# Performance work log

Hardware: AMD Instinct MI355X
Metric: run time of the kernel (lower is better)

## Reference

```python
import jax, jax.numpy as jnp
import numpy as np

B, S, D, H = 2, 2048, 1024, 16
HD = D // H  # head_dim = 64


def setup_inputs() -> dict:
    key = jax.random.key(0)
    ks = jax.random.split(key, 5)
    scale = 1.0 / np.sqrt(D)
    return {
        "x": jax.random.normal(ks[0], (B, S, D), dtype=jnp.float32),
        "attention_mask": jnp.zeros((B, 1, 1, S), dtype=jnp.float32),
        "Wq": jax.random.normal(ks[1], (D, D), dtype=jnp.float32) * scale,
        "Wk": jax.random.normal(ks[2], (D, D), dtype=jnp.float32) * scale,
        "Wv": jax.random.normal(ks[3], (D, D), dtype=jnp.float32) * scale,
        "Wo": jax.random.normal(ks[4], (D, D), dtype=jnp.float32) * scale,
    }


def reference(x, attention_mask, Wq, Wk, Wv, Wo):
    # nn.Linear applies x @ W.T; weights here stored as [out, in]
    q = jnp.einsum("bsd,ed->bse", x, Wq).reshape(B, S, H, HD).transpose(0, 2, 1, 3)
    k = jnp.einsum("bsd,ed->bse", x, Wk).reshape(B, S, H, HD).transpose(0, 2, 1, 3)
    v = jnp.einsum("bsd,ed->bse", x, Wv).reshape(B, S, H, HD).transpose(0, 2, 1, 3)
    scores = jnp.einsum("bhqd,bhkd->bhqk", q, k) / jnp.sqrt(jnp.float32(HD))
    scores = scores + attention_mask  # additive mask, broadcasts [B,1,1,S]
    attn = jax.nn.softmax(scores, axis=-1)  # dropout p=0 (eval) -> identity
    ctx = jnp.einsum("bhqk,bhkd->bhqd", attn, v)
    ctx = ctx.transpose(0, 2, 1, 3).reshape(B, S, D)
    out = jnp.einsum("bsd,ed->bse", ctx, Wo)
    return out
```

## Files before the change

### kernel.cpp

```cpp
#include <hip/hip_runtime.h>
#include <hip/hip_bf16.h>
#include <cstdint>
#include <cstddef>


#define B_  2
#define S_  2048
#define D_  1024
#define H_  16
#define HD_ 64

typedef __bf16 bf16x8 __attribute__((ext_vector_type(8)));
typedef __bf16 bf16x4 __attribute__((ext_vector_type(4)));
typedef float  f32x4  __attribute__((ext_vector_type(4)));

__device__ __forceinline__ void async16(const __bf16* g, const __bf16* l) {
  __builtin_amdgcn_global_load_lds(
      (const __attribute__((address_space(1))) void*)(uintptr_t)g,
      (__attribute__((address_space(3))) void*)(uint32_t)(uintptr_t)l,
      16, 0, 0);
}

__device__ __forceinline__ unsigned cvt_pk_bf16(float lo, float hi) {
  unsigned r;
  asm("v_cvt_pk_bf16_f32 %0, %1, %2" : "=v"(r) : "v"(lo), "v"(hi));
  return r;
}

__global__ __launch_bounds__(256) void cvt_all(const float* __restrict__ x,
    const float* __restrict__ wq, const float* __restrict__ wk,
    const float* __restrict__ wv, const float* __restrict__ wo,
    __bf16* __restrict__ xb, __bf16* __restrict__ wqb, __bf16* __restrict__ wkb,
    __bf16* __restrict__ wvb, __bf16* __restrict__ wob) {
  const int sel = blockIdx.y;
  const float* src; __bf16* dst; int n;
  if      (sel == 0) { src = x;  dst = xb;  n = B_ * S_ * D_; }
  else if (sel == 1) { src = wq; dst = wqb; n = D_ * D_; }
  else if (sel == 2) { src = wk; dst = wkb; n = D_ * D_; }
  else if (sel == 3) { src = wv; dst = wvb; n = D_ * D_; }
  else               { src = wo; dst = wob; n = D_ * D_; }
  for (int i = blockIdx.x * 256 + threadIdx.x; i * 4 < n; i += gridDim.x * 256) {
    const float4 v = *(const float4*)(src + (size_t)i * 4);
    bf16x4 o;
    o[0] = (__bf16)v.x; o[1] = (__bf16)v.y; o[2] = (__bf16)v.z; o[3] = (__bf16)v.w;
    *(bf16x4*)(dst + (size_t)i * 4) = o;
  }
}

template <typename TC>
__device__ __forceinline__ void gemm97_body(const __bf16* __restrict__ A,
                                            const __bf16* __restrict__ Bm,
                                            TC* __restrict__ C,
                                            const int m0, const int n0,
                                            const int N, const int K) {
  __shared__ __align__(16) __bf16 As[128 * 64];
  __shared__ __align__(16) __bf16 Bs[128 * 64];
  const int tid  = threadIdx.x, lane = tid & 63, wave = tid >> 6;
  const int l15  = lane & 15,   quad = lane >> 4;
  const int wr   = wave >> 1,   wc   = wave & 1;
  const int ebase = wave * 2048 + lane * 8;

  f32x4 acc[4][4] = {};
  for (int k0 = 0; k0 < K; k0 += 64) {
#pragma unroll
    for (int i = 0; i < 4; ++i) {
      const int e = ebase + i * 512;
      const int row = e >> 6, col = e & 63;
      async16(A  + (size_t)(m0 + row) * K + k0 + col, As + (wave * 4 + i) * 512);
      async16(Bm + (size_t)(n0 + row) * K + k0 + col, Bs + (wave * 4 + i) * 512);
    }
    __syncthreads();
#pragma unroll
    for (int kk = 0; kk < 2; ++kk) {
      bf16x8 af[4], bfv[4];
#pragma unroll
      for (int rt = 0; rt < 4; ++rt)
        af[rt] = *(const bf16x8*)(As + (wr * 64 + rt * 16 + l15) * 64 + kk * 32 + quad * 8);
#pragma unroll
      for (int ct = 0; ct < 4; ++ct)
        bfv[ct] = *(const bf16x8*)(Bs + (wc * 64 + ct * 16 + l15) * 64 + kk * 32 + quad * 8);
#pragma unroll
      for (int rt = 0; rt < 4; ++rt)
#pragma unroll
        for (int ct = 0; ct < 4; ++ct)
          acc[rt][ct] = __builtin_amdgcn_mfma_f32_16x16x32_bf16(af[rt], bfv[ct], acc[rt][ct], 0, 0, 0);
    }
    __syncthreads();
  }
#pragma unroll
  for (int rt = 0; rt < 4; ++rt)
#pragma unroll
    for (int ct = 0; ct < 4; ++ct)
#pragma unroll
      for (int r = 0; r < 4; ++r) {
        const int row = m0 + wr * 64 + rt * 16 + quad * 4 + r;
        const int col = n0 + wc * 64 + ct * 16 + l15;
        C[(size_t)row * N + col] = (TC)acc[rt][ct][r];
      }
}

__global__ __launch_bounds__(256) void qkv_gemm(const __bf16* __restrict__ xb,
                                                const __bf16* __restrict__ wq,
                                                const __bf16* __restrict__ wk,
                                                const __bf16* __restrict__ wv,
                                                __bf16* __restrict__ qkv) {
  const int sel = blockIdx.x >> 3;
  const __bf16* Bm = (sel == 0) ? wq : (sel == 1) ? wk : wv;
  __bf16* C = qkv + (size_t)sel * ((size_t)B_ * S_ * D_);
  gemm97_body<__bf16>(xb, Bm, C, blockIdx.y * 128, (blockIdx.x & 7) * 128, D_, D_);
}

__global__ __launch_bounds__(256) void o_gemm(const __bf16* __restrict__ cb,
                                              const __bf16* __restrict__ wo,
                                              float* __restrict__ out) {
  gemm97_body<float>(cb, wo, out, blockIdx.y * 128, blockIdx.x * 128, D_, D_);
}

__global__ __launch_bounds__(256) void vtrans(const __bf16* __restrict__ vb,
                                              __bf16* __restrict__ vt) {
  __shared__ __bf16 tbuf[64][72];
  const int tid = threadIdx.x;
  const int s0 = blockIdx.x * 64, bh = blockIdx.y;
  const int b = bh >> 4, h = bh & 15;
  const __bf16* src = vb + ((size_t)b * S_ + s0) * D_ + h * HD_;
#pragma unroll
  for (int i = 0; i < 2; ++i) {
    const int r = i * 32 + (tid >> 3), c8 = (tid & 7) * 8;
    *(bf16x8*)(&tbuf[r][c8]) = *(const bf16x8*)(src + (size_t)r * D_ + c8);
  }
  __syncthreads();
  __bf16* dst = vt + (size_t)bh * HD_ * S_ + s0;
#pragma unroll
  for (int i = 0; i < 2; ++i) {
    const int hd = i * 32 + (tid >> 3), sc = (tid & 7) * 8;
    bf16x8 v;
#pragma unroll
    for (int j = 0; j < 8; ++j) v[j] = tbuf[sc + j][hd];
    *(bf16x8*)(dst + (size_t)hd * S_ + sc) = v;
  }
}

__global__ __launch_bounds__(512, 4) void attn2(const __bf16* __restrict__ Q,
                                                const __bf16* __restrict__ K,
                                                const __bf16* __restrict__ Vt,
                                                const float* __restrict__ mask,
                                                __bf16* __restrict__ O) {
  constexpr int LKT = 72, LVT = 136;
  __shared__ __align__(16) __bf16 kt[128 * LKT];
  __shared__ __align__(16) __bf16 vt[64 * LVT];
  __shared__ __align__(16) float  msk[128];

  const int tid  = threadIdx.x, lane = tid & 63, wave = tid >> 6;
  const int l15  = lane & 15,   quad = lane >> 4;
  const int b = blockIdx.z, h = blockIdx.y, q0 = blockIdx.x * 128;
  const size_t base   = (size_t)b * S_ * D_ + h * HD_;
  const size_t vtbase = (size_t)(b * H_ + h) * HD_ * S_;
  const int qw = q0 + wave * 16;
  constexpr float LOG2E = 1.44269504088896340736f;
  constexpr float SC    = 0.125f * LOG2E;

  bf16x8 qf[2];
#pragma unroll
  for (int kb = 0; kb < 2; ++kb)
    qf[kb] = *(const bf16x8*)(Q + base + (size_t)(qw + l15) * D_ + kb * 32 + quad * 8);

  float m_run = -1e30f, l_run = 0.f;
  f32x4 oacc[4] = {};

  for (int t0 = 0; t0 < S_; t0 += 128) {
    __syncthreads();
#pragma unroll
    for (int i = 0; i < 2; ++i) {
      const int idx = i * 512 + tid;
      { const int row = idx >> 3, c8 = (idx & 7) * 8;
        *(bf16x8*)(kt + row * LKT + c8) =
            *(const bf16x8*)(K + base + (size_t)(t0 + row) * D_ + c8); }
      { const int row = idx >> 4, c8 = (idx & 15) * 8;
        *(bf16x8*)(vt + row * LVT + c8) =
            *(const bf16x8*)(Vt + vtbase + (size_t)row * S_ + t0 + c8); }
    }
    if (tid < 128) msk[tid] = mask[(size_t)b * S_ + t0 + tid] * LOG2E;
    __syncthreads();

    f32x4 sacc[8] = {};
    __builtin_amdgcn_s_setprio(1);
#pragma unroll
    for (int kti = 0; kti < 8; ++kti) {
      const __bf16* kr = kt + (kti * 16 + l15) * LKT + quad * 8;
      const bf16x8 a0 = *(const bf16x8*)(kr);
      const bf16x8 a1 = *(const bf16x8*)(kr + 32);
      sacc[kti] = __builtin_amdgcn_mfma_f32_16x16x32_bf16(a0, qf[0], sacc[kti], 0, 0, 0);
      sacc[kti] = __builtin_amdgcn_mfma_f32_16x16x32_bf16(a1, qf[1], sacc[kti], 0, 0, 0);
    }
    __builtin_amdgcn_s_setprio(0);

    f32x4 tm4;
#pragma unroll
    for (int r = 0; r < 4; ++r) tm4[r] = -1e30f;
#pragma unroll
    for (int kti = 0; kti < 8; ++kti) {
      const f32x4 mv = *(const f32x4*)(msk + kti * 16 + quad * 4);
#pragma unroll
      for (int r = 0; r < 4; ++r) {
        sacc[kti][r] = sacc[kti][r] * SC + mv[r];
        tm4[r] = fmaxf(tm4[r], sacc[kti][r]);
      }
    }
    float tm = fmaxf(fmaxf(tm4[0], tm4[1]), fmaxf(tm4[2], tm4[3]));
    tm = fmaxf(tm, __shfl_xor(tm, 16));
    tm = fmaxf(tm, __shfl_xor(tm, 32));

    if (!__all(tm <= m_run + 8.f)) {
      const float mnew  = fmaxf(m_run, tm);
      const float alpha = __builtin_amdgcn_exp2f(m_run - mnew);
      m_run = mnew;
      l_run *= alpha;
#pragma unroll
      for (int r = 0; r < 4; ++r) {
        const float aR = __shfl(alpha, quad * 4 + r);
#pragma unroll
        for (int nt = 0; nt < 4; ++nt) oacc[nt][r] *= aR;
      }
    }

    float ts = 0.f;
#pragma unroll
    for (int kb = 0; kb < 4; ++kb) {
      unsigned dd[2][2];
#pragma unroll
      for (int kk = 0; kk < 2; ++kk) {
        const int kti = 2 * kb + kk;
        float p[4];
#pragma unroll
        for (int r = 0; r < 4; ++r) {
          p[r] = __builtin_amdgcn_exp2f(sacc[kti][r] - m_run);
          ts += p[r];
        }
        dd[kk][0] = cvt_pk_bf16(p[0], p[1]);
        dd[kk][1] = cvt_pk_bf16(p[2], p[3]);
      }
      unsigned a0 = dd[0][0], b0 = dd[1][0], a1 = dd[0][1], b1 = dd[1][1];
      asm("v_permlane32_swap_b32 %0, %1" : "+v"(a0), "+v"(b0));
      asm("v_permlane16_swap_b32 %0, %1" : "+v"(a0), "+v"(b0));
      asm("v_permlane32_swap_b32 %0, %1" : "+v"(a1), "+v"(b1));
      asm("v_permlane16_swap_b32 %0, %1" : "+v"(a1), "+v"(b1));
      union { unsigned u[4]; bf16x8 v; } pw;
      pw.u[0] = a0; pw.u[1] = a1; pw.u[2] = b0; pw.u[3] = b1;
      const bf16x8 pa = pw.v;
      __builtin_amdgcn_s_setprio(1);
#pragma unroll
      for (int nt = 0; nt < 4; ++nt) {
        const bf16x8 vf = *(const bf16x8*)(vt + (nt * 16 + l15) * LVT + kb * 32 + quad * 8);
        oacc[nt] = __builtin_amdgcn_mfma_f32_16x16x32_bf16(pa, vf, oacc[nt], 0, 0, 0);
      }
      __builtin_amdgcn_s_setprio(0);
    }
    ts += __shfl_xor(ts, 16);
    ts += __shfl_xor(ts, 32);
    l_run += ts;
  }

#pragma unroll
  for (int r = 0; r < 4; ++r) {
    const float lR  = __shfl(l_run, quad * 4 + r);
    const float inv = 1.0f / lR;
    const int row = qw + quad * 4 + r;
#pragma unroll
    for (int nt = 0; nt < 4; ++nt)
      O[base + (size_t)row * D_ + nt * 16 + l15] = (__bf16)(oacc[nt][r] * inv);
  }
}

extern "C" void kernel_launch(void* const* d_in, const int* in_sizes, int n_in,
                              void* d_out, int out_size, void* d_ws, size_t ws_size,
                              hipStream_t stream) {
  const float* x    = (const float*)d_in[0];
  const float* mask = (const float*)d_in[1];
  const float* Wq   = (const float*)d_in[2];
  const float* Wk   = (const float*)d_in[3];
  const float* Wv   = (const float*)d_in[4];
  const float* Wo   = (const float*)d_in[5];

  char* ws = (char*)d_ws;
  const size_t MB = 1ull << 20;
  const size_t NT = (size_t)B_ * S_ * D_;
  __bf16* xb  = (__bf16*)(ws);
  __bf16* wqb = (__bf16*)(ws + 8 * MB);
  __bf16* wkb = (__bf16*)(ws + 10 * MB);
  __bf16* wvb = (__bf16*)(ws + 12 * MB);
  __bf16* wob = (__bf16*)(ws + 14 * MB);
  __bf16* qkv = (__bf16*)(ws + 16 * MB);
  __bf16* qb  = qkv;
  __bf16* kb  = qkv + NT;
  __bf16* vb  = qkv + 2 * NT;
  __bf16* vtb = xb;
  __bf16* cb  = vb;

  cvt_all<<<dim3(1024, 5), 256, 0, stream>>>(x, Wq, Wk, Wv, Wo, xb, wqb, wkb, wvb, wob);
  qkv_gemm<<<dim3(24, 32), 256, 0, stream>>>(xb, wqb, wkb, wvb, qkv);
  vtrans<<<dim3(32, 32), 256, 0, stream>>>(vb, vtb);
  attn2<<<dim3(S_ / 128, H_, B_), 512, 0, stream>>>(qb, kb, vtb, mask, cb);
  o_gemm<<<dim3(8, 32), 256, 0, stream>>>(cb, wob, (float*)d_out);
}
```

Before: 226.9 us.

## Double-buffer K/V tiles with register prefetch and compute row sums via MFMA

```diff
diff --git a/kernel.cpp b/kernel.cpp
--- a/kernel.cpp
+++ b/kernel.cpp
@@ -146,9 +146,9 @@
                                                 const float* __restrict__ mask,
                                                 __bf16* __restrict__ O) {
   constexpr int LKT = 72, LVT = 136;
-  __shared__ __align__(16) __bf16 kt[128 * LKT];
-  __shared__ __align__(16) __bf16 vt[64 * LVT];
-  __shared__ __align__(16) float  msk[128];
+  __shared__ __align__(16) __bf16 kt[2][128 * LKT];
+  __shared__ __align__(16) __bf16 vt[2][64 * LVT];
+  __shared__ __align__(16) float  mfull[S_];
 
   const int tid  = threadIdx.x, lane = tid & 63, wave = tid >> 6;
   const int l15  = lane & 15,   quad = lane >> 4;
@@ -158,35 +158,59 @@
   const int qw = q0 + wave * 16;
   constexpr float LOG2E = 1.44269504088896340736f;
   constexpr float SC    = 0.125f * LOG2E;
+  constexpr int  NT     = S_ / 128;
+
+  const int idx0 = tid,        kr0 = idx0 >> 3, kc0 = (idx0 & 7) * 8;
+  const int idx1 = 512 + tid,  kr1 = idx1 >> 3, kc1 = (idx1 & 7) * 8;
+  const int vr0 = idx0 >> 4, vc0 = (idx0 & 15) * 8;
+  const int vr1 = idx1 >> 4, vc1 = (idx1 & 15) * 8;
 
   bf16x8 qf[2];
 #pragma unroll
   for (int kb = 0; kb < 2; ++kb)
     qf[kb] = *(const bf16x8*)(Q + base + (size_t)(qw + l15) * D_ + kb * 32 + quad * 8);
 
-  float m_run = -1e30f, l_run = 0.f;
+  bf16x8 ones;
+#pragma unroll
+  for (int j = 0; j < 8; ++j) ones[j] = (__bf16)1.0f;
+
+  float m_run = -1e30f;
   f32x4 oacc[4] = {};
-
-  for (int t0 = 0; t0 < S_; t0 += 128) {
-    __syncthreads();
-#pragma unroll
-    for (int i = 0; i < 2; ++i) {
-      const int idx = i * 512 + tid;
-      { const int row = idx >> 3, c8 = (idx & 7) * 8;
-        *(bf16x8*)(kt + row * LKT + c8) =
-            *(const bf16x8*)(K + base + (size_t)(t0 + row) * D_ + c8); }
-      { const int row = idx >> 4, c8 = (idx & 15) * 8;
-        *(bf16x8*)(vt + row * LVT + c8) =
-            *(const bf16x8*)(Vt + vtbase + (size_t)row * S_ + t0 + c8); }
-    }
-    if (tid < 128) msk[tid] = mask[(size_t)b * S_ + t0 + tid] * LOG2E;
-    __syncthreads();
+  f32x4 lacc   = {};
+
+  bf16x8 rk0, rk1, rv0, rv1;
+  rk0 = *(const bf16x8*)(K + base + (size_t)kr0 * D_ + kc0);
+  rk1 = *(const bf16x8*)(K + base + (size_t)kr1 * D_ + kc1);
+  rv0 = *(const bf16x8*)(Vt + vtbase + (size_t)vr0 * S_ + vc0);
+  rv1 = *(const bf16x8*)(Vt + vtbase + (size_t)vr1 * S_ + vc1);
+#pragma unroll
+  for (int i = 0; i < S_ / 512; ++i)
+    mfull[i * 512 + tid] = mask[(size_t)b * S_ + i * 512 + tid] * LOG2E;
+  *(bf16x8*)(&kt[0][kr0 * LKT + kc0]) = rk0;
+  *(bf16x8*)(&kt[0][kr1 * LKT + kc1]) = rk1;
+  *(bf16x8*)(&vt[0][vr0 * LVT + vc0]) = rv0;
+  *(bf16x8*)(&vt[0][vr1 * LVT + vc1]) = rv1;
+  __syncthreads();
+
+  for (int t = 0; t < NT; ++t) {
+    const int cur = t & 1;
+    const int t0  = t * 128;
+    const __bf16* ktb = &kt[cur][0];
+    const __bf16* vtb = &vt[cur][0];
+
+    if (t + 1 < NT) {
+      const int tn = t0 + 128;
+      rk0 = *(const bf16x8*)(K + base + (size_t)(tn + kr0) * D_ + kc0);
+      rk1 = *(const bf16x8*)(K + base + (size_t)(tn + kr1) * D_ + kc1);
+      rv0 = *(const bf16x8*)(Vt + vtbase + (size_t)vr0 * S_ + tn + vc0);
+      rv1 = *(const bf16x8*)(Vt + vtbase + (size_t)vr1 * S_ + tn + vc1);
+    }
 
     f32x4 sacc[8] = {};
     __builtin_amdgcn_s_setprio(1);
 #pragma unroll
     for (int kti = 0; kti < 8; ++kti) {
-      const __bf16* kr = kt + (kti * 16 + l15) * LKT + quad * 8;
+      const __bf16* kr = ktb + (kti * 16 + l15) * LKT + quad * 8;
       const bf16x8 a0 = *(const bf16x8*)(kr);
       const bf16x8 a1 = *(const bf16x8*)(kr + 32);
       sacc[kti] = __builtin_amdgcn_mfma_f32_16x16x32_bf16(a0, qf[0], sacc[kti], 0, 0, 0);
@@ -199,7 +223,7 @@
     for (int r = 0; r < 4; ++r) tm4[r] = -1e30f;
 #pragma unroll
     for (int kti = 0; kti < 8; ++kti) {
-      const f32x4 mv = *(const f32x4*)(msk + kti * 16 + quad * 4);
+      const f32x4 mv = *(const f32x4*)(mfull + t0 + kti * 16 + quad * 4);
 #pragma unroll
       for (int r = 0; r < 4; ++r) {
         sacc[kti][r] = sacc[kti][r] * SC + mv[r];
@@ -214,16 +238,15 @@
       const float mnew  = fmaxf(m_run, tm);
       const float alpha = __builtin_amdgcn_exp2f(m_run - mnew);
       m_run = mnew;
-      l_run *= alpha;
 #pragma unroll
       for (int r = 0; r < 4; ++r) {
         const float aR = __shfl(alpha, quad * 4 + r);
+        lacc[r] *= aR;
 #pragma unroll
         for (int nt = 0; nt < 4; ++nt) oacc[nt][r] *= aR;
       }
     }
 
-    float ts = 0.f;
 #pragma unroll
     for (int kb = 0; kb < 4; ++kb) {
       unsigned dd[2][2];
@@ -232,10 +255,8 @@
         const int kti = 2 * kb + kk;
         float p[4];
 #pragma unroll
-        for (int r = 0; r < 4; ++r) {
+        for (int r = 0; r < 4; ++r)
           p[r] = __builtin_amdgcn_exp2f(sacc[kti][r] - m_run);
-          ts += p[r];
-        }
         dd[kk][0] = cvt_pk_bf16(p[0], p[1]);
         dd[kk][1] = cvt_pk_bf16(p[2], p[3]);
       }
@@ -248,22 +269,29 @@
       pw.u[0] = a0; pw.u[1] = a1; pw.u[2] = b0; pw.u[3] = b1;
       const bf16x8 pa = pw.v;
       __builtin_amdgcn_s_setprio(1);
+      lacc = __builtin_amdgcn_mfma_f32_16x16x32_bf16(pa, ones, lacc, 0, 0, 0);
 #pragma unroll
       for (int nt = 0; nt < 4; ++nt) {
-        const bf16x8 vf = *(const bf16x8*)(vt + (nt * 16 + l15) * LVT + kb * 32 + quad * 8);
+        const bf16x8 vf = *(const bf16x8*)(vtb + (nt * 16 + l15) * LVT + kb * 32 + quad * 8);
         oacc[nt] = __builtin_amdgcn_mfma_f32_16x16x32_bf16(pa, vf, oacc[nt], 0, 0, 0);
       }
       __builtin_amdgcn_s_setprio(0);
     }
-    ts += __shfl_xor(ts, 16);
-    ts += __shfl_xor(ts, 32);
-    l_run += ts;
+
+    __syncthreads();
+    if (t + 1 < NT) {
+      const int nxt = cur ^ 1;
+      *(bf16x8*)(&kt[nxt][kr0 * LKT + kc0]) = rk0;
+      *(bf16x8*)(&kt[nxt][kr1 * LKT + kc1]) = rk1;
+      *(bf16x8*)(&vt[nxt][vr0 * LVT + vc0]) = rv0;
+      *(bf16x8*)(&vt[nxt][vr1 * LVT + vc1]) = rv1;
+    }
+    __syncthreads();
   }
 
 #pragma unroll
   for (int r = 0; r < 4; ++r) {
-    const float lR  = __shfl(l_run, quad * 4 + r);
-    const float inv = 1.0f / lR;
+    const float inv = 1.0f / lacc[r];
     const int row = qw + quad * 4 + r;
 #pragma unroll
     for (int nt = 0; nt < 4; ++nt)
```

Result: faster. 219.2 us (-3.4%).
